# Kernel tuning notes

Hardware: AMD Instinct MI355X
Metric: run time of the kernel (lower is better)

Reference implementation:

```python
import jax, jax.numpy as jnp
import numpy as np

BS, N, NDIMS, HNF, HID = 32, 512, 3, 6, 64
NORM_CONSTANT = 1.0
EPS = 1e-8


def remove_mean_with_mask(x, node_mask):
    n = jnp.sum(node_mask, axis=1, keepdims=True)  # [bs,1,1]
    mean = jnp.sum(x, axis=1, keepdims=True) / n
    return x - mean * node_mask


def setup_inputs() -> dict:
    key = jax.random.key(0)
    k0, k1, k2 = jax.random.split(key, 3)
    xh = jax.random.normal(k0, (BS, N, NDIMS + HNF), dtype=jnp.float32)
    node_mask = jnp.ones((BS, N, 1), dtype=jnp.float32)
    # feature_embedding: Linear(6,64) -> SiLU -> Linear(64,2)
    W1 = jax.random.normal(k1, (HNF, HID), dtype=jnp.float32) * 0.1
    b1 = jnp.zeros((HID,), dtype=jnp.float32)
    W2 = jax.random.normal(k2, (HID, 2), dtype=jnp.float32) * 0.1
    b2 = jnp.zeros((2,), dtype=jnp.float32)
    return {"xh": xh, "node_mask": node_mask, "W1": W1, "b1": b1, "W2": W2, "b2": b2}


def reference(xh, node_mask, W1, b1, W2, b2):
    # x_input = remove_mean_with_mask(xh[..., :3], node_mask)
    x = remove_mean_with_mask(xh[..., :NDIMS], node_mask)  # [bs,n,3]
    # coord2diff over the dense fully-connected edge set (row=i, col=j):
    # coord_diff[b,i,j] = x[b,i] - x[b,j]
    coord_diff = x[:, :, None, :] - x[:, None, :, :]        # [bs,n,n,3]
    radial = jnp.sum(coord_diff ** 2, axis=-1, keepdims=True)  # [bs,n,n,1]
    norm = jnp.sqrt(radial + EPS)
    coord_diff = coord_diff / (norm + NORM_CONSTANT)
    # feature_embedding MLP on node features h = xh[..., 3:]
    h = xh[..., NDIMS:]                                      # [bs,n,6]
    h_emb = jax.nn.silu(h @ W1 + b1) @ W2 + b2               # [bs,n,2]
    # node-pair gather: h_i = h_emb[rows], h_j = h_emb[cols]
    h_i = jnp.broadcast_to(h_emb[:, :, None, :], (BS, N, N, 2))
    h_j = jnp.broadcast_to(h_emb[:, None, :, :], (BS, N, N, 2))
    # edge_features = cat([radial, coord_diff, h_i, h_j], -1) -> [bs,n,n,8]
    edge_features = jnp.concatenate([radial, coord_diff, h_i, h_j], axis=-1)
    return edge_features
```

## Files before the change

### kernel.cpp

```cpp
#include <hip/hip_runtime.h>
#include <math.h>

#define BS 32
#define NN 512
#define NDIMS 3
#define HNF 6
#define HID 64
#define EPSV 1e-8f
#define NORMC 1.0f

__global__ __launch_bounds__(512) void prep_kernel(
    const float* __restrict__ xh,
    const float* __restrict__ mask,
    const float* __restrict__ W1,
    const float* __restrict__ b1,
    const float* __restrict__ W2,
    const float* __restrict__ b2,
    float* __restrict__ xc,
    float* __restrict__ hemb)
{
    const int b = blockIdx.x;
    const int i = threadIdx.x;

    __shared__ float s_red[8][4];
    __shared__ float s_mean[3];
    __shared__ float sW1[HNF * HID];
    __shared__ float sb1[HID];
    __shared__ float sW2[HID * 2];
    __shared__ float sb2[2];

    for (int t = i; t < HNF * HID; t += 512) sW1[t] = W1[t];
    if (i < HID)     sb1[i] = b1[i];
    for (int t = i; t < HID * 2; t += 512) sW2[t] = W2[t];
    if (i < 2)       sb2[i] = b2[i];

    const float* row = xh + ((size_t)b * NN + i) * (NDIMS + HNF);
    float x0 = row[0], x1 = row[1], x2 = row[2];
    float h[HNF];
    #pragma unroll
    for (int k = 0; k < HNF; ++k) h[k] = row[NDIMS + k];
    float m = mask[(size_t)b * NN + i];

    float v0 = x0, v1 = x1, v2 = x2, vm = m;
    #pragma unroll
    for (int off = 32; off > 0; off >>= 1) {
        v0 += __shfl_down(v0, off);
        v1 += __shfl_down(v1, off);
        v2 += __shfl_down(v2, off);
        vm += __shfl_down(vm, off);
    }
    const int lane = i & 63, wave = i >> 6;
    if (lane == 0) {
        s_red[wave][0] = v0; s_red[wave][1] = v1;
        s_red[wave][2] = v2; s_red[wave][3] = vm;
    }
    __syncthreads();
    if (i == 0) {
        float t0 = 0.f, t1 = 0.f, t2 = 0.f, tm = 0.f;
        #pragma unroll
        for (int w = 0; w < 8; ++w) {
            t0 += s_red[w][0]; t1 += s_red[w][1];
            t2 += s_red[w][2]; tm += s_red[w][3];
        }
        s_mean[0] = t0 / tm; s_mean[1] = t1 / tm; s_mean[2] = t2 / tm;
    }
    __syncthreads();

    float cx0 = x0 - s_mean[0] * m;
    float cx1 = x1 - s_mean[1] * m;
    float cx2 = x2 - s_mean[2] * m;
    float* xo = xc + ((size_t)b * NN + i) * 3;
    xo[0] = cx0; xo[1] = cx1; xo[2] = cx2;

    float acc0 = sb2[0], acc1 = sb2[1];
    #pragma unroll 8
    for (int hh = 0; hh < HID; ++hh) {
        float z = sb1[hh];
        #pragma unroll
        for (int k = 0; k < HNF; ++k) z += h[k] * sW1[k * HID + hh];
        float s = z / (1.0f + expf(-z));
        acc0 += s * sW2[hh * 2 + 0];
        acc1 += s * sW2[hh * 2 + 1];
    }
    float* ho = hemb + ((size_t)b * NN + i) * 2;
    ho[0] = acc0; ho[1] = acc1;
}

__global__ __launch_bounds__(512) void edge_kernel(
    const float* __restrict__ xc,
    const float* __restrict__ hemb,
    float4* __restrict__ out4)
{
    const int bi = blockIdx.x;
    const int b  = bi >> 9;
    const int i  = bi & (NN - 1);
    const int j  = threadIdx.x;

    __shared__ float sx[NN * 3];
    __shared__ float sh[NN * 2];

    const float* xb = xc   + (size_t)b * NN * 3;
    const float* hb = hemb + (size_t)b * NN * 2;

    sx[j]           = xb[j];
    sx[j + 512]     = xb[j + 512];
    sx[j + 1024]    = xb[j + 1024];
    sh[j]           = hb[j];
    sh[j + 512]     = hb[j + 512];
    __syncthreads();

    const float xi0 = sx[i * 3 + 0], xi1 = sx[i * 3 + 1], xi2 = sx[i * 3 + 2];
    const float hi0 = sh[i * 2 + 0], hi1 = sh[i * 2 + 1];

    const float xj0 = sx[j * 3 + 0], xj1 = sx[j * 3 + 1], xj2 = sx[j * 3 + 2];
    const float hj0 = sh[j * 2 + 0], hj1 = sh[j * 2 + 1];

    const float d0 = xi0 - xj0;
    const float d1 = xi1 - xj1;
    const float d2 = xi2 - xj2;
    const float radial = d0 * d0 + d1 * d1 + d2 * d2;
    const float norm = sqrtf(radial + EPSV);
    const float inv = 1.0f / (norm + NORMC);

    const size_t e = ((size_t)bi * NN + j) * 2;
    out4[e + 0] = make_float4(radial, d0 * inv, d1 * inv, d2 * inv);
    out4[e + 1] = make_float4(hi0, hi1, hj0, hj1);
}

extern "C" void kernel_launch(void* const* d_in, const int* in_sizes, int n_in,
                              void* d_out, int out_size, void* d_ws, size_t ws_size,
                              hipStream_t stream) {
    const float* xh   = (const float*)d_in[0];
    const float* mask = (const float*)d_in[1];
    const float* W1   = (const float*)d_in[2];
    const float* b1   = (const float*)d_in[3];
    const float* W2   = (const float*)d_in[4];
    const float* b2   = (const float*)d_in[5];

    float* xc   = (float*)d_ws;
    float* hemb = xc + (size_t)BS * NN * 3;

    prep_kernel<<<BS, 512, 0, stream>>>(xh, mask, W1, b1, W2, b2, xc, hemb);
    edge_kernel<<<BS * NN, 512, 0, stream>>>(xc, hemb, (float4*)d_out);
}
```

Baseline: 277.9 us.

## Coalesce edge output stores and process eight rows per block

Remaps threads so adjacent lanes write contiguous float4 halves of each edge record, making stores fully coalesced. Each block now handles eight i-rows, amortizing the shared-memory staging and barrier over more work. Uses hardware rcp/sqrt intrinsics instead of IEEE divide and sqrt. Odd lanes compute geometry they discard, and approximate reciprocal may slightly change precision.

```diff
diff --git a/kernel.cpp b/kernel.cpp
--- a/kernel.cpp
+++ b/kernel.cpp
@@ -8,6 +8,7 @@
 #define HID 64
 #define EPSV 1e-8f
 #define NORMC 1.0f
+#define ROWS 8
 
 __global__ __launch_bounds__(512) void prep_kernel(
     const float* __restrict__ xh,
@@ -30,9 +31,9 @@
     __shared__ float sb2[2];
 
     for (int t = i; t < HNF * HID; t += 512) sW1[t] = W1[t];
-    if (i < HID)     sb1[i] = b1[i];
+    if (i < HID) sb1[i] = b1[i];
     for (int t = i; t < HID * 2; t += 512) sW2[t] = W2[t];
-    if (i < 2)       sb2[i] = b2[i];
+    if (i < 2)   sb2[i] = b2[i];
 
     const float* row = xh + ((size_t)b * NN + i) * (NDIMS + HNF);
     float x0 = row[0], x1 = row[1], x2 = row[2];
@@ -91,40 +92,57 @@
     const float* __restrict__ hemb,
     float4* __restrict__ out4)
 {
-    const int bi = blockIdx.x;
-    const int b  = bi >> 9;
-    const int i  = bi & (NN - 1);
-    const int j  = threadIdx.x;
+    const int blk = blockIdx.x;
+    const int bi0 = blk * ROWS;
+    const int b   = bi0 >> 9;
+    const int i0  = bi0 & (NN - 1);
+    const int j   = threadIdx.x;
 
     __shared__ float sx[NN * 3];
     __shared__ float sh[NN * 2];
 
     const float* xb = xc   + (size_t)b * NN * 3;
     const float* hb = hemb + (size_t)b * NN * 2;
-
-    sx[j]           = xb[j];
-    sx[j + 512]     = xb[j + 512];
-    sx[j + 1024]    = xb[j + 1024];
-    sh[j]           = hb[j];
-    sh[j + 512]     = hb[j + 512];
+    sx[j]        = xb[j];
+    sx[j + 512]  = xb[j + 512];
+    sx[j + 1024] = xb[j + 1024];
+    sh[j]        = hb[j];
+    sh[j + 512]  = hb[j + 512];
     __syncthreads();
 
-    const float xi0 = sx[i * 3 + 0], xi1 = sx[i * 3 + 1], xi2 = sx[i * 3 + 2];
-    const float hi0 = sh[i * 2 + 0], hi1 = sh[i * 2 + 1];
+    const int ja = j >> 1;
+    const int jb = 256 + ja;
+    const bool odd = (j & 1) != 0;
 
-    const float xj0 = sx[j * 3 + 0], xj1 = sx[j * 3 + 1], xj2 = sx[j * 3 + 2];
-    const float hj0 = sh[j * 2 + 0], hj1 = sh[j * 2 + 1];
+    const float xa0 = sx[ja * 3 + 0], xa1 = sx[ja * 3 + 1], xa2 = sx[ja * 3 + 2];
+    const float xb0 = sx[jb * 3 + 0], xb1 = sx[jb * 3 + 1], xb2 = sx[jb * 3 + 2];
+    const float ha0 = sh[ja * 2 + 0], ha1 = sh[ja * 2 + 1];
+    const float hb0 = sh[jb * 2 + 0], hb1 = sh[jb * 2 + 1];
 
-    const float d0 = xi0 - xj0;
-    const float d1 = xi1 - xj1;
-    const float d2 = xi2 - xj2;
-    const float radial = d0 * d0 + d1 * d1 + d2 * d2;
-    const float norm = sqrtf(radial + EPSV);
-    const float inv = 1.0f / (norm + NORMC);
+    float4* rowout = out4 + (size_t)bi0 * NN * 2;
 
-    const size_t e = ((size_t)bi * NN + j) * 2;
-    out4[e + 0] = make_float4(radial, d0 * inv, d1 * inv, d2 * inv);
-    out4[e + 1] = make_float4(hi0, hi1, hj0, hj1);
+    #pragma unroll
+    for (int r = 0; r < ROWS; ++r) {
+        const int i = i0 + r;
+        const float xi0 = sx[i * 3 + 0], xi1 = sx[i * 3 + 1], xi2 = sx[i * 3 + 2];
+        const float hi0 = sh[i * 2 + 0], hi1 = sh[i * 2 + 1];
+
+        float d0 = xi0 - xa0, d1 = xi1 - xa1, d2 = xi2 - xa2;
+        float rada = d0 * d0 + d1 * d1 + d2 * d2;
+        float inva = __builtin_amdgcn_rcpf(__builtin_amdgcn_sqrtf(rada + EPSV) + NORMC);
+        float4 va = odd ? make_float4(hi0, hi1, ha0, ha1)
+                        : make_float4(rada, d0 * inva, d1 * inva, d2 * inva);
+
+        float e0 = xi0 - xb0, e1 = xi1 - xb1, e2 = xi2 - xb2;
+        float radb = e0 * e0 + e1 * e1 + e2 * e2;
+        float invb = __builtin_amdgcn_rcpf(__builtin_amdgcn_sqrtf(radb + EPSV) + NORMC);
+        float4 vb = odd ? make_float4(hi0, hi1, hb0, hb1)
+                        : make_float4(radb, e0 * invb, e1 * invb, e2 * invb);
+
+        rowout[j]       = va;
+        rowout[j + 512] = vb;
+        rowout += NN * 2;
+    }
 }
 
 extern "C" void kernel_launch(void* const* d_in, const int* in_sizes, int n_in,
@@ -141,5 +159,5 @@
     float* hemb = xc + (size_t)BS * NN * 3;
 
     prep_kernel<<<BS, 512, 0, stream>>>(xh, mask, W1, b1, W2, b2, xc, hemb);
-    edge_kernel<<<BS * NN, 512, 0, stream>>>(xc, hemb, (float4*)d_out);
+    edge_kernel<<<BS * NN / ROWS, 512, 0, stream>>>(xc, hemb, (float4*)d_out);
 }
```

New measurement: 276.8 us. No clear change (-0.4%).

## Pad node data to float4 and stream edge output with one float4 per thread

Applied to the files above, without the earlier changes.

Intermediate coordinates and embeddings are padded to 16-byte vectors so each is fetched with a single load. The edge kernel drops the shared-memory staging and barrier. Each thread now writes one float4 slot (geometry or features, chosen by parity) and loops over all 32 batches, giving fully contiguous stores. Sqrt and reciprocal use fast hardware builtins, which trades a little accuracy for fewer instructions. The kernel has half as many lanes doing the math, and per-lane branching on parity causes divergence.

```diff
diff --git a/kernel.cpp b/kernel.cpp
--- a/kernel.cpp
+++ b/kernel.cpp
@@ -3,11 +3,12 @@
 
 #define BS 32
 #define NN 512
-#define NDIMS 3
 #define HNF 6
 #define HID 64
 #define EPSV 1e-8f
 #define NORMC 1.0f
+
+typedef float f32x4 __attribute__((ext_vector_type(4)));
 
 __global__ __launch_bounds__(512) void prep_kernel(
     const float* __restrict__ xh,
@@ -16,8 +17,8 @@
     const float* __restrict__ b1,
     const float* __restrict__ W2,
     const float* __restrict__ b2,
-    float* __restrict__ xc,
-    float* __restrict__ hemb)
+    f32x4* __restrict__ xc4,
+    f32x4* __restrict__ he4)
 {
     const int b = blockIdx.x;
     const int i = threadIdx.x;
@@ -27,18 +28,17 @@
     __shared__ float sW1[HNF * HID];
     __shared__ float sb1[HID];
     __shared__ float sW2[HID * 2];
-    __shared__ float sb2[2];
 
     for (int t = i; t < HNF * HID; t += 512) sW1[t] = W1[t];
     if (i < HID)     sb1[i] = b1[i];
-    for (int t = i; t < HID * 2; t += 512) sW2[t] = W2[t];
-    if (i < 2)       sb2[i] = b2[i];
+    if (i < HID * 2) sW2[i] = W2[i];
+    const float sb2_0 = b2[0], sb2_1 = b2[1];
 
-    const float* row = xh + ((size_t)b * NN + i) * (NDIMS + HNF);
+    const float* row = xh + ((size_t)b * NN + i) * 9;
     float x0 = row[0], x1 = row[1], x2 = row[2];
     float h[HNF];
     #pragma unroll
-    for (int k = 0; k < HNF; ++k) h[k] = row[NDIMS + k];
+    for (int k = 0; k < HNF; ++k) h[k] = row[3 + k];
     float m = mask[(size_t)b * NN + i];
 
     float v0 = x0, v1 = x1, v2 = x2, vm = m;
@@ -66,13 +66,14 @@
     }
     __syncthreads();
 
-    float cx0 = x0 - s_mean[0] * m;
-    float cx1 = x1 - s_mean[1] * m;
-    float cx2 = x2 - s_mean[2] * m;
-    float* xo = xc + ((size_t)b * NN + i) * 3;
-    xo[0] = cx0; xo[1] = cx1; xo[2] = cx2;
+    f32x4 xo;
+    xo.x = x0 - s_mean[0] * m;
+    xo.y = x1 - s_mean[1] * m;
+    xo.z = x2 - s_mean[2] * m;
+    xo.w = 0.f;
+    xc4[(size_t)b * NN + i] = xo;
 
-    float acc0 = sb2[0], acc1 = sb2[1];
+    float acc0 = sb2_0, acc1 = sb2_1;
     #pragma unroll 8
     for (int hh = 0; hh < HID; ++hh) {
         float z = sb1[hh];
@@ -82,49 +83,46 @@
         acc0 += s * sW2[hh * 2 + 0];
         acc1 += s * sW2[hh * 2 + 1];
     }
-    float* ho = hemb + ((size_t)b * NN + i) * 2;
-    ho[0] = acc0; ho[1] = acc1;
+    f32x4 ho; ho.x = acc0; ho.y = acc1; ho.z = 0.f; ho.w = 0.f;
+    he4[(size_t)b * NN + i] = ho;
 }
 
-__global__ __launch_bounds__(512) void edge_kernel(
-    const float* __restrict__ xc,
-    const float* __restrict__ hemb,
-    float4* __restrict__ out4)
+__global__ __launch_bounds__(256) void edge_kernel(
+    const f32x4* __restrict__ xc4,
+    const f32x4* __restrict__ he4,
+    f32x4* __restrict__ out4)
 {
-    const int bi = blockIdx.x;
-    const int b  = bi >> 9;
-    const int i  = bi & (NN - 1);
-    const int j  = threadIdx.x;
+    const int tid = blockIdx.x * 256 + threadIdx.x;
+    const int i   = tid >> 10;
+    const int q   = tid & 1023;
+    const int j   = q >> 1;
+    const bool odd = (q & 1) != 0;
 
-    __shared__ float sx[NN * 3];
-    __shared__ float sh[NN * 2];
+    const f32x4* pj  = (odd ? he4 : xc4) + j;
+    const f32x4* pxi = xc4 + i;
+    const f32x4* phi = he4 + i;
+    f32x4*       po  = out4 + tid;
 
-    const float* xb = xc   + (size_t)b * NN * 3;
-    const float* hb = hemb + (size_t)b * NN * 2;
+    #pragma unroll 4
+    for (int b = 0; b < BS; ++b) {
+        const f32x4 vj = pj [(size_t)b * NN];
+        const f32x4 xi = pxi[(size_t)b * NN];
+        const f32x4 hi = phi[(size_t)b * NN];
 
-    sx[j]           = xb[j];
-    sx[j + 512]     = xb[j + 512];
-    sx[j + 1024]    = xb[j + 1024];
-    sh[j]           = hb[j];
-    sh[j + 512]     = hb[j + 512];
-    __syncthreads();
+        const float d0 = xi.x - vj.x;
+        const float d1 = xi.y - vj.y;
+        const float d2 = xi.z - vj.z;
+        const float rad = d0 * d0 + d1 * d1 + d2 * d2;
+        const float inv = __builtin_amdgcn_rcpf(__builtin_amdgcn_sqrtf(rad + EPSV) + NORMC);
 
-    const float xi0 = sx[i * 3 + 0], xi1 = sx[i * 3 + 1], xi2 = sx[i * 3 + 2];
-    const float hi0 = sh[i * 2 + 0], hi1 = sh[i * 2 + 1];
+        f32x4 o;
+        o.x = odd ? hi.x : rad;
+        o.y = odd ? hi.y : d0 * inv;
+        o.z = odd ? vj.x : d1 * inv;
+        o.w = odd ? vj.y : d2 * inv;
 
-    const float xj0 = sx[j * 3 + 0], xj1 = sx[j * 3 + 1], xj2 = sx[j * 3 + 2];
-    const float hj0 = sh[j * 2 + 0], hj1 = sh[j * 2 + 1];
-
-    const float d0 = xi0 - xj0;
-    const float d1 = xi1 - xj1;
-    const float d2 = xi2 - xj2;
-    const float radial = d0 * d0 + d1 * d1 + d2 * d2;
-    const float norm = sqrtf(radial + EPSV);
-    const float inv = 1.0f / (norm + NORMC);
-
-    const size_t e = ((size_t)bi * NN + j) * 2;
-    out4[e + 0] = make_float4(radial, d0 * inv, d1 * inv, d2 * inv);
-    out4[e + 1] = make_float4(hi0, hi1, hj0, hj1);
+        po[(size_t)b * NN * NN * 2 / 1] = o;
+    }
 }
 
 extern "C" void kernel_launch(void* const* d_in, const int* in_sizes, int n_in,
@@ -137,9 +135,9 @@
     const float* W2   = (const float*)d_in[4];
     const float* b2   = (const float*)d_in[5];
 
-    float* xc   = (float*)d_ws;
-    float* hemb = xc + (size_t)BS * NN * 3;
+    f32x4* xc4 = (f32x4*)d_ws;
+    f32x4* he4 = xc4 + (size_t)BS * NN;
 
-    prep_kernel<<<BS, 512, 0, stream>>>(xh, mask, W1, b1, W2, b2, xc, hemb);
-    edge_kernel<<<BS * NN, 512, 0, stream>>>(xc, hemb, (float4*)d_out);
+    prep_kernel<<<BS, 512, 0, stream>>>(xh, mask, W1, b1, W2, b2, xc4, he4);
+    edge_kernel<<<(BS * NN * NN * 2 / BS) / 256, 256, 0, stream>>>(xc4, he4, (f32x4*)d_out);
 }
```

Result: no change. 280.0 us (+0.7%).
